# Kernel optimization log

Measured on AMD Instinct MI355X. Metric: run time of the kernel, lower is better.

The kernel has to match this reference:

```python
import jax, jax.numpy as jnp
import numpy as np

TOPOLOGY = [-1, 0, 0, 0, 1, 2, 3, 4, 5, 6, 7, 8, 9, 9, 9, 12, 13, 14, 16, 17, 18, 19, 20, 21]
JOINT_WEIGHTS = np.ones(24, dtype=np.float32)
B1 = 1.0
B2 = 1.0


def quaternion_to_matrix(q):
    # pytorch3d convention: real part first (w, x, y, z)
    w, x, y, z = q[..., 0], q[..., 1], q[..., 2], q[..., 3]
    two_s = 2.0 / jnp.sum(q * q, axis=-1)
    o = jnp.stack([
        1 - two_s * (y * y + z * z), two_s * (x * y - z * w), two_s * (x * z + y * w),
        two_s * (x * y + z * w), 1 - two_s * (x * x + z * z), two_s * (y * z - x * w),
        two_s * (x * z - y * w), two_s * (y * z + x * w), 1 - two_s * (x * x + y * y),
    ], axis=-1)
    return o.reshape(q.shape[:-1] + (3, 3))


def fk(topology, X_m, X_t):
    # X_m: (bs, T, J*4+3), X_t: (bs, J, 3)
    J = len(topology)
    quat = X_m[..., :-3].reshape(X_m.shape[:-1] + (J, 4))
    local_rot = quaternion_to_matrix(quat)          # (bs, T, J, 3, 3)
    grots = [None] * J
    gtrs = [None] * J
    grots[0] = local_rot[..., 0, :, :]
    gtrs[0] = X_m[..., -3:]                          # root translation
    for i in range(1, J):
        pi = topology[i]
        grots[i] = jnp.matmul(grots[pi], local_rot[..., i, :, :])
        gtrs[i] = jnp.einsum('btij,bj->bti', grots[pi], X_t[:, i]) + gtrs[pi]
    return jnp.stack(grots, axis=-3), jnp.stack(gtrs, axis=-2)


def split_raw_motion(raw_motion):
    position = raw_motion[..., -3:]
    rotation = raw_motion[..., :-3]
    rotation = rotation.reshape(rotation.shape[:-1] + (-1, 4))
    norm = jnp.linalg.norm(rotation, axis=-1, keepdims=True)
    rotation = rotation / jnp.maximum(norm, 1e-12)
    return rotation, position


def weighted_mse(w, a, b):
    # w: (J,), a/b: (bs, T, J, C) -> per-joint weighted mean squared error
    return jnp.mean(w[None, None, :, None] * (a - b) ** 2)


def setup_inputs() -> dict:
    key = jax.random.key(0)
    k1, k2, k3, k4 = jax.random.split(key, 4)
    bs, T, J = 64, 2048, 24
    return {
        'Y_m': jax.random.normal(k1, (bs, T, J * 4 + 3), dtype=jnp.float32),
        'X_m': jax.random.normal(k2, (bs, T, J * 4 + 3), dtype=jnp.float32),
        'Y_t': jax.random.normal(k3, (bs, J, 3), dtype=jnp.float32),
        'X_t': jax.random.normal(k4, (bs, J, 3), dtype=jnp.float32),
    }


def reference(Y_m, X_m, Y_t, X_t):
    w = jnp.asarray(JOINT_WEIGHTS)
    rot_x, pos_x = split_raw_motion(X_m)
    rot_y, pos_y = split_raw_motion(Y_m)
    grot_y, gtr_y = fk(TOPOLOGY, Y_m, Y_t)
    grot_x, gtr_x = fk(TOPOLOGY, X_m, X_t)
    loss_rot = B1 * weighted_mse(w, rot_y, rot_x)
    loss_fk = B2 * (2.5 * weighted_mse(w, gtr_y, gtr_x)
                    + jnp.mean((pos_y - pos_x) ** 2))
    return loss_rot + loss_fk
```

## Files before the change

### kernel.cpp

```cpp
#include <hip/hip_runtime.h>

#define BS 64
#define TT 2048
#define NJ 24
#define ROWF 99
#define BLOCK 256
#define NROWS (BS * TT)
#define PFD 8

__device__ __forceinline__ float4 ld4u(const float* __restrict__ p) {
  return *reinterpret_cast<const float4*>(p);
}

__device__ __forceinline__ void quat2mat_s(float w, float x, float y, float z,
                                           float s, float* R) {
  const float xx = s*x*x, yy = s*y*y, zz = s*z*z;
  const float xy = s*x*y, xz = s*x*z, yz = s*y*z;
  const float xw = s*x*w, yw = s*y*w, zw = s*z*w;
  R[0] = 1.0f - (yy+zz); R[1] = xy - zw;        R[2] = xz + yw;
  R[3] = xy + zw;        R[4] = 1.0f - (xx+zz); R[5] = yz - xw;
  R[6] = xz - yw;        R[7] = yz + xw;        R[8] = 1.0f - (xx+yy);
}

__device__ __forceinline__ void mm3(const float* A, const float* B, float* C) {
#pragma unroll
  for (int r = 0; r < 3; ++r) {
#pragma unroll
    for (int c = 0; c < 3; ++c) {
      C[3*r+c] = fmaf(A[3*r], B[c], fmaf(A[3*r+1], B[3+c], A[3*r+2]*B[6+c]));
    }
  }
}

__global__ __launch_bounds__(BLOCK, 2) void motion_loss_kernel(
    const float* __restrict__ Ym, const float* __restrict__ Xm,
    const float* __restrict__ Yt, const float* __restrict__ Xt,
    float* __restrict__ out) {
  const int tid = threadIdx.x;
  const size_t row = (size_t)blockIdx.x * BLOCK + tid;
  const int b = (int)(row / TT);
  const float* __restrict__ xr = Xm + row * ROWF;
  const float* __restrict__ yr = Ym + row * ROWF;
  const float* __restrict__ tX = Xt + (size_t)b * NJ * 3;
  const float* __restrict__ tY = Yt + (size_t)b * NJ * 3;

  float GX[3][9], GY[3][9], D[3][3];
  float rot_acc = 0.0f, gtr_acc = 0.0f, pos_acc = 0.0f;

  const float4 posx = ld4u(xr + 95);
  const float4 posy = ld4u(yr + 95);
  float4 qx[PFD], qy[PFD];
#pragma unroll
  for (int k = 0; k < PFD; ++k) { qx[k] = ld4u(xr + 4*k); qy[k] = ld4u(yr + 4*k); }

  {
    const float4 vx = qx[0], vy = qy[0];
    qx[0] = ld4u(xr + 4*PFD); qy[0] = ld4u(yr + 4*PFD);
    const float qqx = vx.x*vx.x + vx.y*vx.y + vx.z*vx.z + vx.w*vx.w;
    const float qqy = vy.x*vy.x + vy.y*vy.y + vy.z*vy.z + vy.w*vy.w;
    const float ix = 1.0f / fmaxf(sqrtf(qqx), 1e-12f);
    const float iy = 1.0f / fmaxf(sqrtf(qqy), 1e-12f);
    const float r0 = vy.x*iy - vx.x*ix, r1 = vy.y*iy - vx.y*ix;
    const float r2 = vy.z*iy - vx.z*ix, r3 = vy.w*iy - vx.w*ix;
    rot_acc += r0*r0 + r1*r1 + r2*r2 + r3*r3;
    quat2mat_s(vx.x, vx.y, vx.z, vx.w, 2.0f / qqx, GX[0]);
    quat2mat_s(vy.x, vy.y, vy.z, vy.w, 2.0f / qqy, GY[0]);
    D[0][0] = posy.y - posx.y; D[0][1] = posy.z - posx.z; D[0][2] = posy.w - posx.w;
    const float dd = D[0][0]*D[0][0] + D[0][1]*D[0][1] + D[0][2]*D[0][2];
    gtr_acc += dd;
    pos_acc  = dd;
  }

#define JSTEP(j, PS, NS) do {                                                  \
    const float4 vx = qx[(j) & (PFD-1)], vy = qy[(j) & (PFD-1)];               \
    if ((j) + PFD < NJ) {                                                      \
      qx[(j) & (PFD-1)] = ld4u(xr + 4*((j) + PFD));                            \
      qy[(j) & (PFD-1)] = ld4u(yr + 4*((j) + PFD));                            \
    }                                                                          \
    const float qqx = vx.x*vx.x + vx.y*vx.y + vx.z*vx.z + vx.w*vx.w;           \
    const float qqy = vy.x*vy.x + vy.y*vy.y + vy.z*vy.z + vy.w*vy.w;           \
    const float ix = 1.0f / fmaxf(sqrtf(qqx), 1e-12f);                         \
    const float iy = 1.0f / fmaxf(sqrtf(qqy), 1e-12f);                         \
    const float r0 = vy.x*iy - vx.x*ix, r1 = vy.y*iy - vx.y*ix;                \
    const float r2 = vy.z*iy - vx.z*ix, r3 = vy.w*iy - vx.w*ix;                \
    rot_acc += r0*r0 + r1*r1 + r2*r2 + r3*r3;                                  \
    const float tx0 = tX[3*(j)], tx1 = tX[3*(j)+1], tx2 = tX[3*(j)+2];         \
    const float ty0 = tY[3*(j)], ty1 = tY[3*(j)+1], ty2 = tY[3*(j)+2];         \
    const float vx0 = fmaf(GX[PS][0],tx0, fmaf(GX[PS][1],tx1, GX[PS][2]*tx2)); \
    const float vx1 = fmaf(GX[PS][3],tx0, fmaf(GX[PS][4],tx1, GX[PS][5]*tx2)); \
    const float vx2 = fmaf(GX[PS][6],tx0, fmaf(GX[PS][7],tx1, GX[PS][8]*tx2)); \
    const float vy0 = fmaf(GY[PS][0],ty0, fmaf(GY[PS][1],ty1, GY[PS][2]*ty2)); \
    const float vy1 = fmaf(GY[PS][3],ty0, fmaf(GY[PS][4],ty1, GY[PS][5]*ty2)); \
    const float vy2 = fmaf(GY[PS][6],ty0, fmaf(GY[PS][7],ty1, GY[PS][8]*ty2)); \
    const float d0 = D[PS][0] + (vy0 - vx0);                                   \
    const float d1 = D[PS][1] + (vy1 - vx1);                                   \
    const float d2 = D[PS][2] + (vy2 - vx2);                                   \
    gtr_acc += d0*d0 + d1*d1 + d2*d2;                                          \
    float RX[9], RY[9], GnX[9], GnY[9];                                        \
    quat2mat_s(vx.x, vx.y, vx.z, vx.w, 2.0f / qqx, RX);                        \
    quat2mat_s(vy.x, vy.y, vy.z, vy.w, 2.0f / qqy, RY);                        \
    mm3(GX[PS], RX, GnX);                                                      \
    mm3(GY[PS], RY, GnY);                                                      \
    _Pragma("unroll")                                                          \
    for (int k = 0; k < 9; ++k) { GX[NS][k] = GnX[k]; GY[NS][k] = GnY[k]; }    \
    D[NS][0] = d0; D[NS][1] = d1; D[NS][2] = d2;                               \
  } while (0)

  JSTEP( 1, 0, 1); JSTEP( 2, 0, 2); JSTEP( 3, 0, 0);
  JSTEP( 4, 1, 1); JSTEP( 5, 2, 2); JSTEP( 6, 0, 0);
  JSTEP( 7, 1, 1); JSTEP( 8, 2, 2); JSTEP( 9, 0, 0);
  JSTEP(10, 1, 1); JSTEP(11, 2, 2);
  JSTEP(12, 0, 1); JSTEP(13, 0, 2); JSTEP(14, 0, 0);
  JSTEP(15, 1, 1); JSTEP(16, 2, 2); JSTEP(17, 0, 0);
  JSTEP(18, 2, 2); JSTEP(19, 0, 0); JSTEP(20, 2, 2);
  JSTEP(21, 0, 0); JSTEP(22, 2, 2); JSTEP(23, 0, 0);
#undef JSTEP

  const float c_rot = 1.0f / ((float)NROWS * NJ * 4);
  const float c_gtr = 2.5f / ((float)NROWS * NJ * 3);
  const float c_pos = 1.0f / ((float)NROWS * 3);
  float contrib = c_rot * rot_acc + c_gtr * gtr_acc + c_pos * pos_acc;
#pragma unroll
  for (int o = 32; o > 0; o >>= 1) contrib += __shfl_down(contrib, o, 64);
  if ((tid & 63) == 0) atomicAdd(out, contrib);
}

extern "C" void kernel_launch(void* const* d_in, const int* in_sizes, int n_in,
                              void* d_out, int out_size, void* d_ws, size_t ws_size,
                              hipStream_t stream) {
  const float* Ym = (const float*)d_in[0];
  const float* Xm = (const float*)d_in[1];
  const float* Yt = (const float*)d_in[2];
  const float* Xt = (const float*)d_in[3];
  float* out = (float*)d_out;
  hipMemsetAsync(out, 0, sizeof(float), stream);
  motion_loss_kernel<<<NROWS / BLOCK, BLOCK, 0, stream>>>(Ym, Xm, Yt, Xt, out);
}
```

Measured before the change: 158.6 us.

## Stage quaternion windows through double-buffered LDS with cooperative coalesced loads

Instead of each thread streaming its own 99-float row with per-thread float4 loads, the block cooperatively loads 16-float windows (four joints) for all its rows into double-buffered shared memory. Each wavefront then reads contiguous 64-byte segments per row, and the compute loop reads quaternions from LDS. The next window is issued while the current one is processed. The block size is halved to 128 to match. This aims to improve global load coalescing and cache-line use, at the cost of two barriers per window and extra LDS traffic.

```diff
diff --git a/kernel.cpp b/kernel.cpp
--- a/kernel.cpp
+++ b/kernel.cpp
@@ -4,9 +4,9 @@
 #define TT 2048
 #define NJ 24
 #define ROWF 99
-#define BLOCK 256
+#define BLOCK 128
 #define NROWS (BS * TT)
-#define PFD 8
+#define LSTR 20
 
 __device__ __forceinline__ float4 ld4u(const float* __restrict__ p) {
   return *reinterpret_cast<const float4*>(p);
@@ -36,26 +36,51 @@
     const float* __restrict__ Ym, const float* __restrict__ Xm,
     const float* __restrict__ Yt, const float* __restrict__ Xt,
     float* __restrict__ out) {
-  const int tid = threadIdx.x;
-  const size_t row = (size_t)blockIdx.x * BLOCK + tid;
-  const int b = (int)(row / TT);
-  const float* __restrict__ xr = Xm + row * ROWF;
-  const float* __restrict__ yr = Ym + row * ROWF;
+  __shared__ __align__(16) float lX[2][BLOCK * LSTR];
+  __shared__ __align__(16) float lY[2][BLOCK * LSTR];
+
+  const int t = threadIdx.x;
+  const size_t row0 = (size_t)blockIdx.x * BLOCK;
+  const int b = blockIdx.x >> 4;
+  const float* __restrict__ xt = Xm + row0 * ROWF;
+  const float* __restrict__ yt = Ym + row0 * ROWF;
   const float* __restrict__ tX = Xt + (size_t)b * NJ * 3;
   const float* __restrict__ tY = Yt + (size_t)b * NJ * 3;
+
+  const float4 posx = ld4u(xt + t * ROWF + 95);
+  const float4 posy = ld4u(yt + t * ROWF + 95);
+
+  float4 sx[4], sy[4];
+
+#define STAGE_ISSUE(w) do {                                                    \
+    _Pragma("unroll")                                                          \
+    for (int k = 0; k < 4; ++k) {                                              \
+      const int l = t + k * BLOCK, r = l >> 2, s = l & 3;                      \
+      sx[k] = ld4u(xt + r * ROWF + (w) * 16 + s * 4);                          \
+      sy[k] = ld4u(yt + r * ROWF + (w) * 16 + s * 4);                          \
+    }                                                                          \
+  } while (0)
+
+#define STAGE_WRITE(w) do {                                                    \
+    _Pragma("unroll")                                                          \
+    for (int k = 0; k < 4; ++k) {                                              \
+      const int l = t + k * BLOCK, r = l >> 2, s = l & 3;                      \
+      *reinterpret_cast<float4*>(&lX[(w) & 1][r * LSTR + s * 4]) = sx[k];      \
+      *reinterpret_cast<float4*>(&lY[(w) & 1][r * LSTR + s * 4]) = sy[k];      \
+    }                                                                          \
+  } while (0)
+
+  STAGE_ISSUE(0);
+  STAGE_WRITE(0);
+  STAGE_ISSUE(1);
+  __syncthreads();
 
   float GX[3][9], GY[3][9], D[3][3];
   float rot_acc = 0.0f, gtr_acc = 0.0f, pos_acc = 0.0f;
 
-  const float4 posx = ld4u(xr + 95);
-  const float4 posy = ld4u(yr + 95);
-  float4 qx[PFD], qy[PFD];
-#pragma unroll
-  for (int k = 0; k < PFD; ++k) { qx[k] = ld4u(xr + 4*k); qy[k] = ld4u(yr + 4*k); }
-
   {
-    const float4 vx = qx[0], vy = qy[0];
-    qx[0] = ld4u(xr + 4*PFD); qy[0] = ld4u(yr + 4*PFD);
+    const float4 vx = *reinterpret_cast<const float4*>(&lX[0][t * LSTR]);
+    const float4 vy = *reinterpret_cast<const float4*>(&lY[0][t * LSTR]);
     const float qqx = vx.x*vx.x + vx.y*vx.y + vx.z*vx.z + vx.w*vx.w;
     const float qqy = vy.x*vy.x + vy.y*vy.y + vy.z*vy.z + vy.w*vy.w;
     const float ix = 1.0f / fmaxf(sqrtf(qqx), 1e-12f);
@@ -72,11 +97,10 @@
   }
 
 #define JSTEP(j, PS, NS) do {                                                  \
-    const float4 vx = qx[(j) & (PFD-1)], vy = qy[(j) & (PFD-1)];               \
-    if ((j) + PFD < NJ) {                                                      \
-      qx[(j) & (PFD-1)] = ld4u(xr + 4*((j) + PFD));                            \
-      qy[(j) & (PFD-1)] = ld4u(yr + 4*((j) + PFD));                            \
-    }                                                                          \
+    const float4 vx = *reinterpret_cast<const float4*>(                        \
+        &lX[((j) >> 2) & 1][t * LSTR + ((j) & 3) * 4]);                        \
+    const float4 vy = *reinterpret_cast<const float4*>(                        \
+        &lY[((j) >> 2) & 1][t * LSTR + ((j) & 3) * 4]);                        \
     const float qqx = vx.x*vx.x + vx.y*vx.y + vx.z*vx.z + vx.w*vx.w;           \
     const float qqy = vy.x*vy.x + vy.y*vy.y + vy.z*vy.z + vy.w*vy.w;           \
     const float ix = 1.0f / fmaxf(sqrtf(qqx), 1e-12f);                         \
@@ -106,15 +130,28 @@
     D[NS][0] = d0; D[NS][1] = d1; D[NS][2] = d2;                               \
   } while (0)
 
+#define BOUNDARY(wnext, wissue) do {                                           \
+    __syncthreads();                                                           \
+    STAGE_WRITE(wnext);                                                        \
+    if ((wissue) < 6) STAGE_ISSUE(wissue);                                     \
+    __syncthreads();                                                           \
+  } while (0)
+
   JSTEP( 1, 0, 1); JSTEP( 2, 0, 2); JSTEP( 3, 0, 0);
-  JSTEP( 4, 1, 1); JSTEP( 5, 2, 2); JSTEP( 6, 0, 0);
-  JSTEP( 7, 1, 1); JSTEP( 8, 2, 2); JSTEP( 9, 0, 0);
-  JSTEP(10, 1, 1); JSTEP(11, 2, 2);
-  JSTEP(12, 0, 1); JSTEP(13, 0, 2); JSTEP(14, 0, 0);
-  JSTEP(15, 1, 1); JSTEP(16, 2, 2); JSTEP(17, 0, 0);
-  JSTEP(18, 2, 2); JSTEP(19, 0, 0); JSTEP(20, 2, 2);
-  JSTEP(21, 0, 0); JSTEP(22, 2, 2); JSTEP(23, 0, 0);
+  BOUNDARY(1, 2);
+  JSTEP( 4, 1, 1); JSTEP( 5, 2, 2); JSTEP( 6, 0, 0); JSTEP( 7, 1, 1);
+  BOUNDARY(2, 3);
+  JSTEP( 8, 2, 2); JSTEP( 9, 0, 0); JSTEP(10, 1, 1); JSTEP(11, 2, 2);
+  BOUNDARY(3, 4);
+  JSTEP(12, 0, 1); JSTEP(13, 0, 2); JSTEP(14, 0, 0); JSTEP(15, 1, 1);
+  BOUNDARY(4, 5);
+  JSTEP(16, 2, 2); JSTEP(17, 0, 0); JSTEP(18, 2, 2); JSTEP(19, 0, 0);
+  BOUNDARY(5, 6);
+  JSTEP(20, 2, 2); JSTEP(21, 0, 0); JSTEP(22, 2, 2); JSTEP(23, 0, 0);
 #undef JSTEP
+#undef BOUNDARY
+#undef STAGE_ISSUE
+#undef STAGE_WRITE
 
   const float c_rot = 1.0f / ((float)NROWS * NJ * 4);
   const float c_gtr = 2.5f / ((float)NROWS * NJ * 3);
@@ -122,7 +159,7 @@
   float contrib = c_rot * rot_acc + c_gtr * gtr_acc + c_pos * pos_acc;
 #pragma unroll
   for (int o = 32; o > 0; o >>= 1) contrib += __shfl_down(contrib, o, 64);
-  if ((tid & 63) == 0) atomicAdd(out, contrib);
+  if ((t & 63) == 0) atomicAdd(out, contrib);
 }
 
 extern "C" void kernel_launch(void* const* d_in, const int* in_sizes, int n_in,
```

New measurement: 155.0 us. 2.3% less time.

## Split X and Y forward kinematics across two wavefronts with LDS handoff

Applied to the files above, without the earlier changes.

Each block now handles 64 rows with two wavefronts: one runs forward kinematics on X, the other on Y, and the X results (normalized quats and global translations) are passed through double-buffered shared memory in windows of four joints, with the Y wave lagging one window behind. This halves per-thread register state, aiming for higher occupancy and memory-level parallelism. The normalization switches to rsqrt and the translation accumulation is folded into FMAs. In exchange it adds six block-wide barriers, shared-memory traffic, and a serialized pipeline start and end where only one wave works.

```diff
diff --git a/kernel.cpp b/kernel.cpp
--- a/kernel.cpp
+++ b/kernel.cpp
@@ -4,9 +4,9 @@
 #define TT 2048
 #define NJ 24
 #define ROWF 99
-#define BLOCK 256
+#define BLOCK 128
+#define RPB 64
 #define NROWS (BS * TT)
-#define PFD 8
 
 __device__ __forceinline__ float4 ld4u(const float* __restrict__ p) {
   return *reinterpret_cast<const float4*>(p);
@@ -32,89 +32,107 @@
   }
 }
 
-__global__ __launch_bounds__(BLOCK, 2) void motion_loss_kernel(
+__global__ __launch_bounds__(BLOCK, 4) void motion_loss_kernel(
     const float* __restrict__ Ym, const float* __restrict__ Xm,
     const float* __restrict__ Yt, const float* __restrict__ Xt,
     float* __restrict__ out) {
+  __shared__ float4 hq[2][4][RPB];
+  __shared__ float4 hg[2][4][RPB];
+
   const int tid = threadIdx.x;
-  const size_t row = (size_t)blockIdx.x * BLOCK + tid;
-  const int b = (int)(row / TT);
-  const float* __restrict__ xr = Xm + row * ROWF;
-  const float* __restrict__ yr = Ym + row * ROWF;
-  const float* __restrict__ tX = Xt + (size_t)b * NJ * 3;
-  const float* __restrict__ tY = Yt + (size_t)b * NJ * 3;
+  const int t = tid & 63;
+  const int side = tid >> 6;
+  const size_t row = (size_t)blockIdx.x * RPB + t;
+  const int b = blockIdx.x >> 5;
+  const float* __restrict__ mr = (side ? Ym : Xm) + row * ROWF;
+  const float* __restrict__ tv = (side ? Yt : Xt) + (size_t)b * NJ * 3;
 
-  float GX[3][9], GY[3][9], D[3][3];
+  float4 ring[8];
+#pragma unroll
+  for (int k = 0; k < 8; ++k) ring[k] = ld4u(mr + 4 * k);
+  const float4 pos = ld4u(mr + 95);
+
+  float G[3][9], T[3][3];
   float rot_acc = 0.0f, gtr_acc = 0.0f, pos_acc = 0.0f;
 
-  const float4 posx = ld4u(xr + 95);
-  const float4 posy = ld4u(yr + 95);
-  float4 qx[PFD], qy[PFD];
-#pragma unroll
-  for (int k = 0; k < PFD; ++k) { qx[k] = ld4u(xr + 4*k); qy[k] = ld4u(yr + 4*k); }
-
-  {
-    const float4 vx = qx[0], vy = qy[0];
-    qx[0] = ld4u(xr + 4*PFD); qy[0] = ld4u(yr + 4*PFD);
-    const float qqx = vx.x*vx.x + vx.y*vx.y + vx.z*vx.z + vx.w*vx.w;
-    const float qqy = vy.x*vy.x + vy.y*vy.y + vy.z*vy.z + vy.w*vy.w;
-    const float ix = 1.0f / fmaxf(sqrtf(qqx), 1e-12f);
-    const float iy = 1.0f / fmaxf(sqrtf(qqy), 1e-12f);
-    const float r0 = vy.x*iy - vx.x*ix, r1 = vy.y*iy - vx.y*ix;
-    const float r2 = vy.z*iy - vx.z*ix, r3 = vy.w*iy - vx.w*ix;
-    rot_acc += r0*r0 + r1*r1 + r2*r2 + r3*r3;
-    quat2mat_s(vx.x, vx.y, vx.z, vx.w, 2.0f / qqx, GX[0]);
-    quat2mat_s(vy.x, vy.y, vy.z, vy.w, 2.0f / qqy, GY[0]);
-    D[0][0] = posy.y - posx.y; D[0][1] = posy.z - posx.z; D[0][2] = posy.w - posx.w;
-    const float dd = D[0][0]*D[0][0] + D[0][1]*D[0][1] + D[0][2]*D[0][2];
-    gtr_acc += dd;
-    pos_acc  = dd;
-  }
-
-#define JSTEP(j, PS, NS) do {                                                  \
-    const float4 vx = qx[(j) & (PFD-1)], vy = qy[(j) & (PFD-1)];               \
-    if ((j) + PFD < NJ) {                                                      \
-      qx[(j) & (PFD-1)] = ld4u(xr + 4*((j) + PFD));                            \
-      qy[(j) & (PFD-1)] = ld4u(yr + 4*((j) + PFD));                            \
+#define ROOTSTEP do {                                                          \
+    const float4 q = ring[0]; ring[0] = ld4u(mr + 32);                         \
+    const float qq = q.x*q.x + q.y*q.y + q.z*q.z + q.w*q.w;                    \
+    const float inv = rsqrtf(fmaxf(qq, 1e-24f));                               \
+    const float4 nq = make_float4(q.x*inv, q.y*inv, q.z*inv, q.w*inv);         \
+    quat2mat_s(q.x, q.y, q.z, q.w, 2.0f*inv*inv, G[0]);                        \
+    T[0][0] = pos.y; T[0][1] = pos.z; T[0][2] = pos.w;                         \
+    if (side == 0) {                                                           \
+      hq[0][0][t] = nq;                                                        \
+      hg[0][0][t] = make_float4(pos.y, pos.z, pos.w, 0.0f);                    \
+    } else {                                                                   \
+      const float4 nx = hq[0][0][t];                                           \
+      const float r0 = nq.x-nx.x, r1 = nq.y-nx.y, r2 = nq.z-nx.z, r3 = nq.w-nx.w; \
+      rot_acc += r0*r0 + r1*r1 + r2*r2 + r3*r3;                                \
+      const float4 gx = hg[0][0][t];                                           \
+      const float d0 = pos.y-gx.x, d1 = pos.z-gx.y, d2 = pos.w-gx.z;           \
+      const float dd = d0*d0 + d1*d1 + d2*d2;                                  \
+      gtr_acc += dd; pos_acc = dd;                                             \
     }                                                                          \
-    const float qqx = vx.x*vx.x + vx.y*vx.y + vx.z*vx.z + vx.w*vx.w;           \
-    const float qqy = vy.x*vy.x + vy.y*vy.y + vy.z*vy.z + vy.w*vy.w;           \
-    const float ix = 1.0f / fmaxf(sqrtf(qqx), 1e-12f);                         \
-    const float iy = 1.0f / fmaxf(sqrtf(qqy), 1e-12f);                         \
-    const float r0 = vy.x*iy - vx.x*ix, r1 = vy.y*iy - vx.y*ix;                \
-    const float r2 = vy.z*iy - vx.z*ix, r3 = vy.w*iy - vx.w*ix;                \
-    rot_acc += r0*r0 + r1*r1 + r2*r2 + r3*r3;                                  \
-    const float tx0 = tX[3*(j)], tx1 = tX[3*(j)+1], tx2 = tX[3*(j)+2];         \
-    const float ty0 = tY[3*(j)], ty1 = tY[3*(j)+1], ty2 = tY[3*(j)+2];         \
-    const float vx0 = fmaf(GX[PS][0],tx0, fmaf(GX[PS][1],tx1, GX[PS][2]*tx2)); \
-    const float vx1 = fmaf(GX[PS][3],tx0, fmaf(GX[PS][4],tx1, GX[PS][5]*tx2)); \
-    const float vx2 = fmaf(GX[PS][6],tx0, fmaf(GX[PS][7],tx1, GX[PS][8]*tx2)); \
-    const float vy0 = fmaf(GY[PS][0],ty0, fmaf(GY[PS][1],ty1, GY[PS][2]*ty2)); \
-    const float vy1 = fmaf(GY[PS][3],ty0, fmaf(GY[PS][4],ty1, GY[PS][5]*ty2)); \
-    const float vy2 = fmaf(GY[PS][6],ty0, fmaf(GY[PS][7],ty1, GY[PS][8]*ty2)); \
-    const float d0 = D[PS][0] + (vy0 - vx0);                                   \
-    const float d1 = D[PS][1] + (vy1 - vx1);                                   \
-    const float d2 = D[PS][2] + (vy2 - vx2);                                   \
-    gtr_acc += d0*d0 + d1*d1 + d2*d2;                                          \
-    float RX[9], RY[9], GnX[9], GnY[9];                                        \
-    quat2mat_s(vx.x, vx.y, vx.z, vx.w, 2.0f / qqx, RX);                        \
-    quat2mat_s(vy.x, vy.y, vy.z, vy.w, 2.0f / qqy, RY);                        \
-    mm3(GX[PS], RX, GnX);                                                      \
-    mm3(GY[PS], RY, GnY);                                                      \
-    _Pragma("unroll")                                                          \
-    for (int k = 0; k < 9; ++k) { GX[NS][k] = GnX[k]; GY[NS][k] = GnY[k]; }    \
-    D[NS][0] = d0; D[NS][1] = d1; D[NS][2] = d2;                               \
   } while (0)
 
-  JSTEP( 1, 0, 1); JSTEP( 2, 0, 2); JSTEP( 3, 0, 0);
-  JSTEP( 4, 1, 1); JSTEP( 5, 2, 2); JSTEP( 6, 0, 0);
-  JSTEP( 7, 1, 1); JSTEP( 8, 2, 2); JSTEP( 9, 0, 0);
-  JSTEP(10, 1, 1); JSTEP(11, 2, 2);
-  JSTEP(12, 0, 1); JSTEP(13, 0, 2); JSTEP(14, 0, 0);
-  JSTEP(15, 1, 1); JSTEP(16, 2, 2); JSTEP(17, 0, 0);
-  JSTEP(18, 2, 2); JSTEP(19, 0, 0); JSTEP(20, 2, 2);
-  JSTEP(21, 0, 0); JSTEP(22, 2, 2); JSTEP(23, 0, 0);
+#define JSTEP(j, PS, NS, WPAR) do {                                            \
+    const float4 q = ring[(j) & 7];                                            \
+    if ((j) + 8 < NJ) ring[(j) & 7] = ld4u(mr + 4*((j) + 8));                  \
+    const float qq = q.x*q.x + q.y*q.y + q.z*q.z + q.w*q.w;                    \
+    const float inv = rsqrtf(fmaxf(qq, 1e-24f));                               \
+    const float4 nq = make_float4(q.x*inv, q.y*inv, q.z*inv, q.w*inv);         \
+    const float t0 = tv[3*(j)], t1 = tv[3*(j)+1], t2 = tv[3*(j)+2];            \
+    const float v0 = fmaf(G[PS][0],t0, fmaf(G[PS][1],t1, fmaf(G[PS][2],t2, T[PS][0]))); \
+    const float v1 = fmaf(G[PS][3],t0, fmaf(G[PS][4],t1, fmaf(G[PS][5],t2, T[PS][1]))); \
+    const float v2 = fmaf(G[PS][6],t0, fmaf(G[PS][7],t1, fmaf(G[PS][8],t2, T[PS][2]))); \
+    float R[9], Gn[9];                                                         \
+    quat2mat_s(q.x, q.y, q.z, q.w, 2.0f*inv*inv, R);                           \
+    mm3(G[PS], R, Gn);                                                         \
+    _Pragma("unroll")                                                          \
+    for (int k = 0; k < 9; ++k) G[NS][k] = Gn[k];                              \
+    T[NS][0] = v0; T[NS][1] = v1; T[NS][2] = v2;                               \
+    if (side == 0) {                                                           \
+      hq[WPAR][(j) & 3][t] = nq;                                               \
+      hg[WPAR][(j) & 3][t] = make_float4(v0, v1, v2, 0.0f);                    \
+    } else {                                                                   \
+      const float4 nx = hq[WPAR][(j) & 3][t];                                  \
+      const float r0 = nq.x-nx.x, r1 = nq.y-nx.y, r2 = nq.z-nx.z, r3 = nq.w-nx.w; \
+      rot_acc += r0*r0 + r1*r1 + r2*r2 + r3*r3;                                \
+      const float4 gx = hg[WPAR][(j) & 3][t];                                  \
+      const float d0 = v0-gx.x, d1 = v1-gx.y, d2 = v2-gx.z;                    \
+      gtr_acc += d0*d0 + d1*d1 + d2*d2;                                        \
+    }                                                                          \
+  } while (0)
+
+#define WIN0 do { ROOTSTEP; JSTEP( 1,0,1,0); JSTEP( 2,0,2,0); JSTEP( 3,0,0,0); } while (0)
+#define WIN1 do { JSTEP( 4,1,1,1); JSTEP( 5,2,2,1); JSTEP( 6,0,0,1); JSTEP( 7,1,1,1); } while (0)
+#define WIN2 do { JSTEP( 8,2,2,0); JSTEP( 9,0,0,0); JSTEP(10,1,1,0); JSTEP(11,2,2,0); } while (0)
+#define WIN3 do { JSTEP(12,0,1,1); JSTEP(13,0,2,1); JSTEP(14,0,0,1); JSTEP(15,1,1,1); } while (0)
+#define WIN4 do { JSTEP(16,2,2,0); JSTEP(17,0,0,0); JSTEP(18,2,2,0); JSTEP(19,0,0,0); } while (0)
+#define WIN5 do { JSTEP(20,2,2,1); JSTEP(21,0,0,1); JSTEP(22,2,2,1); JSTEP(23,0,0,1); } while (0)
+
+  if (side == 0) { WIN0; }
+  __syncthreads();
+  if (side == 0) { WIN1; } else { WIN0; }
+  __syncthreads();
+  if (side == 0) { WIN2; } else { WIN1; }
+  __syncthreads();
+  if (side == 0) { WIN3; } else { WIN2; }
+  __syncthreads();
+  if (side == 0) { WIN4; } else { WIN3; }
+  __syncthreads();
+  if (side == 0) { WIN5; } else { WIN4; }
+  __syncthreads();
+  if (side == 1) { WIN5; }
+#undef WIN0
+#undef WIN1
+#undef WIN2
+#undef WIN3
+#undef WIN4
+#undef WIN5
 #undef JSTEP
+#undef ROOTSTEP
 
   const float c_rot = 1.0f / ((float)NROWS * NJ * 4);
   const float c_gtr = 2.5f / ((float)NROWS * NJ * 3);
@@ -122,7 +140,7 @@
   float contrib = c_rot * rot_acc + c_gtr * gtr_acc + c_pos * pos_acc;
 #pragma unroll
   for (int o = 32; o > 0; o >>= 1) contrib += __shfl_down(contrib, o, 64);
-  if ((tid & 63) == 0) atomicAdd(out, contrib);
+  if (side == 1 && t == 0) atomicAdd(out, contrib);
 }
 
 extern "C" void kernel_launch(void* const* d_in, const int* in_sizes, int n_in,
@@ -134,5 +152,5 @@
   const float* Xt = (const float*)d_in[3];
   float* out = (float*)d_out;
   hipMemsetAsync(out, 0, sizeof(float), stream);
-  motion_loss_kernel<<<NROWS / BLOCK, BLOCK, 0, stream>>>(Ym, Xm, Yt, Xt, out);
+  motion_loss_kernel<<<NROWS / RPB, BLOCK, 0, stream>>>(Ym, Xm, Yt, Xt, out);
 }
```

After: 233.6 us. 1.47x slower.
